# Kernel tuning notes

Measured on AMD Instinct MI355X. Metric: run time of the kernel, lower is better.

Reference implementation:

```python
import jax, jax.numpy as jnp
import numpy as np

GMAX = 1.0   # args.gmax
GMIN = 0.01  # args.gmin
EPS = 0.1    # args.e_train


def setup_inputs() -> dict:
    key = jax.random.key(0)
    k1, k2, k3, k4 = jax.random.split(key, 4)
    N, B, NIN, NOUT, E = 8, 32, 128, 128, 1024
    # analog signals live in [0, 1]
    a_previous = jax.random.uniform(k1, (N, B, NIN, E), dtype=jnp.float32)
    # conductance params (clamped to [-gmax, gmax] in forward)
    theta = jax.random.uniform(k2, (NIN + 2, NOUT), dtype=jnp.float32) * 2.0 - 1.0
    # per-replica multiplicative noise seed in [0, 1); forward maps to 1 +- eps
    noise = jax.random.uniform(k3, (N, NIN + 2, NOUT), dtype=jnp.float32)
    # printed-tanh activation params eta = [offset, scale, shift, slope]
    eta = jnp.array([0.0, 1.0, 0.0, 1.0], dtype=jnp.float32) + 0.1 * jax.random.normal(k4, (4,), dtype=jnp.float32)
    return {"a_previous": a_previous, "theta": theta, "noise": noise, "eta": eta}


def reference(a_previous, theta, noise, eta):
    sg = jax.lax.stop_gradient
    # theta property: clamp + gmin pruning with straight-through estimator
    t = jnp.clip(theta, -GMAX, GMAX)
    t = jnp.where(jnp.abs(t) < GMIN, 0.0, t)
    theta_eff = sg(t) + theta - sg(theta)
    # theta_noisy: replicate over N with multiplicative uniform noise in [1-eps, 1+eps]
    theta_noisy = theta_eff[None, :, :] * ((noise * 2.0 - 1.0) * EPS + 1.0)  # [N, M, O], M = n_in+2
    # W: abs-normalized conductances per output column group
    abs_tn = jnp.abs(theta_noisy)
    W = abs_tn / (jnp.sum(abs_tn, axis=1, keepdims=True) + 1e-10)
    # sign masks (constants w.r.t. grad: values fully overwritten in torch)
    pos = sg((theta_noisy >= 0.0).astype(theta_noisy.dtype))
    neg = 1.0 - pos
    # a: [N, B, n_in, E] -> [N, B, E, n_in]; append ones and zeros columns
    a_r = jnp.transpose(a_previous, (0, 1, 3, 2))
    ones = jnp.ones(a_r.shape[:3] + (1,), a_r.dtype)
    zeros = jnp.zeros_like(ones)
    a_ext = jnp.concatenate([a_r, ones, zeros], axis=3)  # [N, B, E, M]
    # INV: unipolar complement; zero the last (zeros) column after inversion
    a_neg = (1.0 - a_ext).at[..., -1].set(0.0)
    # split-sign MAC: z [N, B, E, n_out]
    z = (jnp.einsum('nbem,nmo->nbeo', a_ext, W * pos)
         + jnp.einsum('nbem,nmo->nbeo', a_neg, W * neg))
    # printed tanh activation
    act = eta[0] + eta[1] * jnp.tanh((z - eta[2]) * eta[3])
    # back to [N, B, n_out, E]
    return jnp.transpose(act, (0, 1, 3, 2))
```

## Files before the change

kernel.cpp:

```cpp
#include <hip/hip_runtime.h>
#include <hip/hip_bf16.h>
#include <stdint.h>

#define N_REP 8
#define BATCH 32
#define NIN   128
#define NOUT  128
#define EDIM  1024
#define MDIM  130
#define ETILE 64
#define SE    68

typedef __attribute__((ext_vector_type(8))) short short8;
typedef __attribute__((ext_vector_type(4))) float f32x4;

__device__ __forceinline__ unsigned short f2bf(float f) {
    union { float f; uint32_t u; } v;
    v.f = f;
    uint32_t u = v.u;
    uint32_t r = u + 0x7fffu + ((u >> 16) & 1u);
    return (unsigned short)(r >> 16);
}

__device__ __forceinline__ uint32_t pk2bf(float lo, float hi) {
    __hip_bfloat162 h = __float22bfloat162_rn(make_float2(lo, hi));
    uint32_t d;
    __builtin_memcpy(&d, &h, 4);
    return d;
}

__global__ __launch_bounds__(64)
void prep_kernel(const float* __restrict__ theta,
                 const float* __restrict__ noise,
                 unsigned short* __restrict__ Sg,
                 float* __restrict__ biasg) {
    const int n = blockIdx.x >> 7;
    const int o = blockIdx.x & 127;
    const int lane = threadIdx.x;

    const float* nb = noise + (size_t)n * MDIM * NOUT + o;
    auto tn_at = [&](int m) -> float {
        float t = theta[m * NOUT + o];
        t = fminf(fmaxf(t, -1.f), 1.f);
        if (fabsf(t) < 0.01f) t = 0.f;
        return t * fmaf(nb[m * NOUT], 0.2f, 0.9f);
    };

    const float t0 = tn_at(lane);
    const float t1 = tn_at(lane + 64);
    const float t2 = (lane < 2) ? tn_at(128 + lane) : 0.f;

    float s = fabsf(t0) + fabsf(t1) + fabsf(t2);
#pragma unroll
    for (int d = 1; d < 64; d <<= 1) s += __shfl_xor(s, d, 64);
    const float inv = 1.f / (s + 1e-10f);

    const float w0 = fabsf(t0) * inv, w1 = fabsf(t1) * inv;
    unsigned short* srow = Sg + ((size_t)n * NOUT + o) * NIN;
    srow[lane]      = f2bf(t0 >= 0.f ? w0 : -w0);
    srow[lane + 64] = f2bf(t1 >= 0.f ? w1 : -w1);

    float b = (t0 < 0.f ? w0 : 0.f) + (t1 < 0.f ? w1 : 0.f);
    if (lane == 0 && t2 >= 0.f) b += fabsf(t2) * inv;
#pragma unroll
    for (int d = 1; d < 64; d <<= 1) b += __shfl_xor(b, d, 64);
    if (lane == 0) biasg[n * NOUT + o] = b;
}

__global__ __launch_bounds__(128, 4)
void gemm_kernel(const float* __restrict__ a,
                 const unsigned short* __restrict__ Sg,
                 const float* __restrict__ biasg,
                 const float* __restrict__ eta,
                 float* __restrict__ out) {
    __shared__ uint32_t Alds[64 * SE];
    const int bid  = blockIdx.x;
    const int et   = bid & 15;
    const int nb   = bid >> 4;
    const int n    = nb >> 5;
    const int tid  = threadIdx.x;
    const int lane = tid & 63;
    const int w    = tid >> 6;
    const int r    = lane & 15;
    const int q    = lane >> 4;

    {
        const float* abase = a + (size_t)nb * (NIN * EDIM) + et * ETILE;
        const int e4  = (tid & 15) << 2;
        const int mp0 = tid >> 4;
        float4 va[8], vb[8];
#pragma unroll
        for (int it = 0; it < 8; ++it) {
            const int mp = mp0 + (it << 3);
            va[it] = *(const float4*)(abase + (size_t)(2 * mp) * EDIM + e4);
            vb[it] = *(const float4*)(abase + (size_t)(2 * mp + 1) * EDIM + e4);
        }
#pragma unroll
        for (int it = 0; it < 8; ++it) {
            const int mp = mp0 + (it << 3);
            uint4 d;
            d.x = pk2bf(va[it].x, vb[it].x);
            d.y = pk2bf(va[it].y, vb[it].y);
            d.z = pk2bf(va[it].z, vb[it].z);
            d.w = pk2bf(va[it].w, vb[it].w);
            *(uint4*)&Alds[mp * SE + e4] = d;
        }
    }
    __syncthreads();

    const int o_base = w << 6;

    float e0 = eta[0], e1 = eta[1], e2 = eta[2], e3 = eta[3];
    asm volatile("" : "+v"(e0), "+v"(e1), "+v"(e2), "+v"(e3));
    float bl[4];
#pragma unroll
    for (int fo = 0; fo < 4; ++fo)
        bl[fo] = biasg[n * NOUT + o_base + (fo << 4) + r];

    f32x4 acc[4][4];
#pragma unroll
    for (int fo = 0; fo < 4; ++fo)
#pragma unroll
        for (int fe = 0; fe < 4; ++fe)
            acc[fo][fe] = (f32x4){0.f, 0.f, 0.f, 0.f};

    const unsigned short* sbase = Sg + ((size_t)(n * NOUT) << 7) + (q << 3);
#pragma unroll
    for (int ks = 0; ks < 4; ++ks) {
        short8 sf[4];
#pragma unroll
        for (int fo = 0; fo < 4; ++fo)
            sf[fo] = *(const short8*)(sbase + ((size_t)(o_base + (fo << 4) + r) << 7)
                                             + (ks << 5));
        const int mpb = (ks << 4) + (q << 2);
        short8 af[4];
#pragma unroll
        for (int fe = 0; fe < 4; ++fe) {
            uint32_t d[4];
#pragma unroll
            for (int jj = 0; jj < 4; ++jj)
                d[jj] = Alds[(mpb + jj) * SE + (fe << 4) + r];
            __builtin_memcpy(&af[fe], d, 16);
        }
#pragma unroll
        for (int fo = 0; fo < 4; ++fo)
#pragma unroll
            for (int fe = 0; fe < 4; ++fe)
                acc[fo][fe] = __builtin_amdgcn_mfma_f32_16x16x32_bf16(
                    af[fe], sf[fo], acc[fo][fe], 0, 0, 0);
    }

    float* obase = out + (size_t)nb * (NOUT * EDIM) + et * ETILE;
#pragma unroll
    for (int fo = 0; fo < 4; ++fo) {
        float* orow = obase + (size_t)(o_base + (fo << 4) + r) * EDIM;
        const float bv = bl[fo];
#pragma unroll
        for (int fe = 0; fe < 4; ++fe) {
            f32x4 res;
#pragma unroll
            for (int i = 0; i < 4; ++i) {
                const float z = acc[fo][fe][i] + bv;
                const float y = (z - e2) * e3;
                const float ex = __expf(2.f * y);
                const float th = 1.f - 2.f * __builtin_amdgcn_rcpf(ex + 1.f);
                res[i] = fmaf(e1, th, e0);
            }
            *(f32x4*)(orow + (fe << 4) + (q << 2)) = res;
        }
    }
}

extern "C" void kernel_launch(void* const* d_in, const int* in_sizes, int n_in,
                              void* d_out, int out_size, void* d_ws, size_t ws_size,
                              hipStream_t stream) {
    const float* a     = (const float*)d_in[0];
    const float* theta = (const float*)d_in[1];
    const float* noise = (const float*)d_in[2];
    const float* eta   = (const float*)d_in[3];
    float* out = (float*)d_out;

    unsigned short* Sg = (unsigned short*)d_ws;
    float* biasg = (float*)((char*)d_ws + (size_t)N_REP * NOUT * NIN * sizeof(unsigned short));

    prep_kernel<<<N_REP * NOUT, 64, 0, stream>>>(theta, noise, Sg, biasg);
    gemm_kernel<<<N_REP * BATCH * (EDIM / ETILE), 128, 0, stream>>>(a, Sg, biasg, eta, out);
}
```

Before: 258.2 us.

## Load activations straight from global into MFMA fragments, dropping the LDS staging

The gemm kernel no longer stages the activation tile in shared memory. Each wave now loads its own 32-column E slice from global memory directly into registers, converts to bf16 and feeds the MFMA, and covers all 128 outputs per wave instead of 64. This removes the LDS write/read round trip and the block barrier, and grows blocks to 256 threads covering 128 E columns. The cost is that the scalar global loads are only 16 lanes (64 bytes) contiguous along E, and the 128 weight columns are reloaded per wave with more registers per thread.

```diff
diff --git a/kernel.cpp b/kernel.cpp
--- a/kernel.cpp
+++ b/kernel.cpp
@@ -8,8 +8,6 @@
 #define NOUT  128
 #define EDIM  1024
 #define MDIM  130
-#define ETILE 64
-#define SE    68
 
 typedef __attribute__((ext_vector_type(8))) short short8;
 typedef __attribute__((ext_vector_type(4))) float f32x4;
@@ -67,96 +65,80 @@
     if (lane == 0) biasg[n * NOUT + o] = b;
 }
 
-__global__ __launch_bounds__(128, 4)
+__global__ __launch_bounds__(256, 3)
 void gemm_kernel(const float* __restrict__ a,
                  const unsigned short* __restrict__ Sg,
                  const float* __restrict__ biasg,
                  const float* __restrict__ eta,
                  float* __restrict__ out) {
-    __shared__ uint32_t Alds[64 * SE];
     const int bid  = blockIdx.x;
-    const int et   = bid & 15;
-    const int nb   = bid >> 4;
-    const int n    = nb >> 5;
     const int tid  = threadIdx.x;
     const int lane = tid & 63;
-    const int w    = tid >> 6;
+    const int wv   = tid >> 6;
     const int r    = lane & 15;
     const int q    = lane >> 4;
+    const int nb   = bid >> 3;
+    const int n    = nb >> 5;
+    const int e0w  = (((bid & 7) << 2) | wv) << 5;
 
-    {
-        const float* abase = a + (size_t)nb * (NIN * EDIM) + et * ETILE;
-        const int e4  = (tid & 15) << 2;
-        const int mp0 = tid >> 4;
-        float4 va[8], vb[8];
-#pragma unroll
-        for (int it = 0; it < 8; ++it) {
-            const int mp = mp0 + (it << 3);
-            va[it] = *(const float4*)(abase + (size_t)(2 * mp) * EDIM + e4);
-            vb[it] = *(const float4*)(abase + (size_t)(2 * mp + 1) * EDIM + e4);
-        }
-#pragma unroll
-        for (int it = 0; it < 8; ++it) {
-            const int mp = mp0 + (it << 3);
-            uint4 d;
-            d.x = pk2bf(va[it].x, vb[it].x);
-            d.y = pk2bf(va[it].y, vb[it].y);
-            d.z = pk2bf(va[it].z, vb[it].z);
-            d.w = pk2bf(va[it].w, vb[it].w);
-            *(uint4*)&Alds[mp * SE + e4] = d;
-        }
-    }
-    __syncthreads();
-
-    const int o_base = w << 6;
+    const float* abase = a + (size_t)nb * (NIN * EDIM) + e0w + r;
 
     float e0 = eta[0], e1 = eta[1], e2 = eta[2], e3 = eta[3];
     asm volatile("" : "+v"(e0), "+v"(e1), "+v"(e2), "+v"(e3));
-    float bl[4];
+
+    float bl[8];
 #pragma unroll
-    for (int fo = 0; fo < 4; ++fo)
-        bl[fo] = biasg[n * NOUT + o_base + (fo << 4) + r];
+    for (int fo = 0; fo < 8; ++fo)
+        bl[fo] = biasg[n * NOUT + (fo << 4) + r];
 
-    f32x4 acc[4][4];
+    f32x4 acc[8][2];
 #pragma unroll
-    for (int fo = 0; fo < 4; ++fo)
+    for (int fo = 0; fo < 8; ++fo)
 #pragma unroll
-        for (int fe = 0; fe < 4; ++fe)
+        for (int fe = 0; fe < 2; ++fe)
             acc[fo][fe] = (f32x4){0.f, 0.f, 0.f, 0.f};
 
     const unsigned short* sbase = Sg + ((size_t)(n * NOUT) << 7) + (q << 3);
+
 #pragma unroll
     for (int ks = 0; ks < 4; ++ks) {
-        short8 sf[4];
+        float av[2][8];
 #pragma unroll
-        for (int fo = 0; fo < 4; ++fo)
-            sf[fo] = *(const short8*)(sbase + ((size_t)(o_base + (fo << 4) + r) << 7)
-                                             + (ks << 5));
-        const int mpb = (ks << 4) + (q << 2);
-        short8 af[4];
+        for (int fe = 0; fe < 2; ++fe)
 #pragma unroll
-        for (int fe = 0; fe < 4; ++fe) {
+            for (int j = 0; j < 8; ++j)
+                av[fe][j] = abase[(size_t)((ks << 5) + (q << 3) + j) * EDIM + (fe << 4)];
+
+        short8 sf[8];
+#pragma unroll
+        for (int fo = 0; fo < 8; ++fo)
+            sf[fo] = *(const short8*)(sbase + ((size_t)((fo << 4) + r) << 7) + (ks << 5));
+
+        short8 af[2];
+#pragma unroll
+        for (int fe = 0; fe < 2; ++fe) {
             uint32_t d[4];
 #pragma unroll
-            for (int jj = 0; jj < 4; ++jj)
-                d[jj] = Alds[(mpb + jj) * SE + (fe << 4) + r];
+            for (int t = 0; t < 4; ++t)
+                d[t] = pk2bf(av[fe][2 * t], av[fe][2 * t + 1]);
             __builtin_memcpy(&af[fe], d, 16);
         }
+
 #pragma unroll
-        for (int fo = 0; fo < 4; ++fo)
+        for (int fo = 0; fo < 8; ++fo)
 #pragma unroll
-            for (int fe = 0; fe < 4; ++fe)
+            for (int fe = 0; fe < 2; ++fe)
                 acc[fo][fe] = __builtin_amdgcn_mfma_f32_16x16x32_bf16(
                     af[fe], sf[fo], acc[fo][fe], 0, 0, 0);
     }
 
-    float* obase = out + (size_t)nb * (NOUT * EDIM) + et * ETILE;
+    float* obase = out + (size_t)nb * (NOUT * EDIM) + e0w;
 #pragma unroll
-    for (int fo = 0; fo < 4; ++fo) {
-        float* orow = obase + (size_t)(o_base + (fo << 4) + r) * EDIM;
+    for (int fo = 0; fo < 8; ++fo) {
+        float* orow = obase + (size_t)((fo << 4) + r) * EDIM;
         const float bv = bl[fo];
 #pragma unroll
-        for (int fe = 0; fe < 4; ++fe) {
+        for (int fe = 0; fe < 2; ++fe) {
             f32x4 res;
 #pragma unroll
             for (int i = 0; i < 4; ++i) {
@@ -184,5 +166,5 @@
     float* biasg = (float*)((char*)d_ws + (size_t)N_REP * NOUT * NIN * sizeof(unsigned short));
 
     prep_kernel<<<N_REP * NOUT, 64, 0, stream>>>(theta, noise, Sg, biasg);
-    gemm_kernel<<<N_REP * BATCH * (EDIM / ETILE), 128, 0, stream>>>(a, Sg, biasg, eta, out);
+    gemm_kernel<<<N_REP * BATCH * 8, 256, 0, stream>>>(a, Sg, biasg, eta, out);
 }
```

Measured after the change: 268.6 us. 1.04x slower.
